# Kernel optimization log

Hardware: AMD Instinct MI355X
Metric: run time of the kernel (lower is better)

The kernel has to match this reference:

```python
import jax, jax.numpy as jnp
import numpy as np

DIM = 768
HEADS = 12
HEAD_DIM = DIM // HEADS
EPS = 1e-5


def _layernorm(x, w, b):
    # normalize over last axis (head_dim), affine params shape [head_dim]
    mu = jnp.mean(x, axis=-1, keepdims=True)
    var = jnp.mean(jnp.square(x - mu), axis=-1, keepdims=True)
    return (x - mu) * jax.lax.rsqrt(var + EPS) * w + b


def setup_inputs() -> dict:
    key = jax.random.key(0)
    ks = jax.random.split(key, 8)
    B, N, C = 8, 1024, DIM
    s = 1.0 / np.sqrt(C)
    return {
        "x": jax.random.normal(ks[0], (B, N, C), jnp.float32),
        "qkv_w": jax.random.normal(ks[1], (3 * C, C), jnp.float32) * s,
        "qkv_b": jnp.zeros((3 * C,), jnp.float32),
        "qn_w": jnp.ones((HEAD_DIM,), jnp.float32),
        "qn_b": jnp.zeros((HEAD_DIM,), jnp.float32),
        "kn_w": jnp.ones((HEAD_DIM,), jnp.float32),
        "kn_b": jnp.zeros((HEAD_DIM,), jnp.float32),
        "proj_w": jax.random.normal(ks[2], (C, C), jnp.float32) * s,
        "proj_b": jnp.zeros((C,), jnp.float32),
    }


def reference(x, qkv_w, qkv_b, qn_w, qn_b, kn_w, kn_b, proj_w, proj_b):
    B, N, C = x.shape
    H, D = HEADS, HEAD_DIM
    scale = D ** -0.5
    # qkv projection: [B,N,3C] -> [3,B,H,N,D]
    qkv = (x @ qkv_w.T + qkv_b).reshape(B, N, 3, H, D).transpose(2, 0, 3, 1, 4)
    q, k, v = qkv[0], qkv[1], qkv[2]
    q = _layernorm(q, qn_w, qn_b)
    k = _layernorm(k, kn_w, kn_b)
    # attention scores [B,H,N,N]
    attn = jnp.einsum("bhqd,bhkd->bhqk", q, k) * scale
    attn = jax.nn.softmax(attn, axis=-1)
    out = jnp.einsum("bhqk,bhkd->bhqd", attn, v)  # [B,H,N,D]
    out = out.transpose(0, 2, 1, 3).reshape(B, N, C)
    return out @ proj_w.T + proj_b
```

## Files before the change

### kernel.cpp

```cpp
#include <hip/hip_runtime.h>

#define DIM 768
#define HEADS 12
#define HDIM 64
#define B_ 8
#define N_ 1024
#define EPS 1e-5f
#define QPRE 0.18033688f

typedef __bf16 bf16x8 __attribute__((ext_vector_type(8)));
typedef float  f32x4  __attribute__((ext_vector_type(4)));

using u16 = unsigned short;
using u32 = unsigned int;

static __device__ __forceinline__ u16 f2b_rne(float f){
    u32 u = __float_as_uint(f);
    u += 0x7fffu + ((u >> 16) & 1u);
    return (u16)(u >> 16);
}

static __device__ __forceinline__ u32 cvt_pk_bf16(float lo, float hi){
    u32 r;
    asm("v_cvt_pk_bf16_f32 %0, %1, %2" : "=v"(r) : "v"(lo), "v"(hi));
    return r;
}

static __device__ __forceinline__ void gl_lds16(const void* g, void* l){
    __builtin_amdgcn_global_load_lds(
        (const __attribute__((address_space(1))) unsigned int*)g,
        (__attribute__((address_space(3))) unsigned int*)l, 16, 0, 0);
}

__global__ __launch_bounds__(256) void cast3_kernel(
    const float* __restrict__ s0, u16* __restrict__ d0, int n0,
    const float* __restrict__ s1, u16* __restrict__ d1, int n1,
    const float* __restrict__ s2, u16* __restrict__ d2, int n2)
{
    int i = blockIdx.x * 256 + threadIdx.x;
    const float* s; u16* d;
    if (i < n0)            { s = s0; d = d0; }
    else if (i < n0 + n1)  { s = s1; d = d1; i -= n0; }
    else if (i < n0+n1+n2) { s = s2; d = d2; i -= n0 + n1; }
    else return;
    const float4* p = (const float4*)s;
    float4 a = p[2*i], b = p[2*i+1];
    uint4 r;
    r.x = (u32)f2b_rne(a.x) | ((u32)f2b_rne(a.y) << 16);
    r.y = (u32)f2b_rne(a.z) | ((u32)f2b_rne(a.w) << 16);
    r.z = (u32)f2b_rne(b.x) | ((u32)f2b_rne(b.y) << 16);
    r.w = (u32)f2b_rne(b.z) | ((u32)f2b_rne(b.w) << 16);
    ((uint4*)d)[i] = r;
}

__global__ __launch_bounds__(256) void qkv_gemm_ln(
    const u16* __restrict__ xb, const u16* __restrict__ wb,
    const float* __restrict__ bias,
    const float* __restrict__ qn_w, const float* __restrict__ qn_b,
    const float* __restrict__ kn_w, const float* __restrict__ kn_b,
    u16* __restrict__ Q, u16* __restrict__ K, u16* __restrict__ VT)
{
    __shared__ __align__(16) unsigned char Asl[2][128*128];
    __shared__ __align__(16) unsigned char Bsl[2][128*128];
    const int t = threadIdx.x;
    const int lane = t & 63, wid = t >> 6;
    const int wr = wid >> 1, wc = wid & 1;
    const int l15 = lane & 15, l4 = lane >> 4;
    const int lr  = lane >> 3;
    const int lcs = ((lane & 7) ^ lr & 7) * 16;
    const int rsw = (l15 & 7) << 4;

    const int b0 = blockIdx.x;
    const int lg = (b0 & 7) * 144 + (b0 >> 3);
    const int col0 = (lg % 18) * 128, row0 = (lg / 18) * 128;

    f32x4 acc[4][4];
    #pragma unroll
    for (int m = 0; m < 4; ++m)
        #pragma unroll
        for (int n = 0; n < 4; ++n) acc[m][n] = f32x4{0.f,0.f,0.f,0.f};

    const unsigned char* aSrc = (const unsigned char*)xb + (size_t)(row0 + lr)*1536 + lcs;
    const unsigned char* bSrc = (const unsigned char*)wb + (size_t)(col0 + lr)*1536 + lcs;

    auto stage = [&](int buf, int k0s){
        #pragma unroll
        for (int c = 0; c < 4; ++c) {
            int rg = wid*32 + c*8;
            gl_lds16(aSrc + (size_t)rg*1536 + k0s*2, Asl[buf] + rg*128);
            gl_lds16(bSrc + (size_t)rg*1536 + k0s*2, Bsl[buf] + rg*128);
        }
    };

    stage(0, 0);

    for (int step = 0; step < 12; ++step) {
        const int cur = step & 1;
        if (step < 11) {
            stage(cur ^ 1, (step + 1) * 64);
            asm volatile("s_waitcnt vmcnt(8)" ::: "memory");
        } else {
            asm volatile("s_waitcnt vmcnt(0)" ::: "memory");
        }
        __builtin_amdgcn_s_barrier();

        #pragma unroll
        for (int s = 0; s < 2; ++s) {
            bf16x8 af[4], bfr[4];
            #pragma unroll
            for (int m = 0; m < 4; ++m)
                af[m] = *(const bf16x8*)(Asl[cur] + (wr*64 + m*16 + l15)*128 + ((l4*16 + s*64) ^ rsw));
            #pragma unroll
            for (int n = 0; n < 4; ++n)
                bfr[n] = *(const bf16x8*)(Bsl[cur] + (wc*64 + n*16 + l15)*128 + ((l4*16 + s*64) ^ rsw));
            #pragma unroll
            for (int m = 0; m < 4; ++m)
                #pragma unroll
                for (int n = 0; n < 4; ++n)
                    acc[m][n] = __builtin_amdgcn_mfma_f32_16x16x32_bf16(af[m], bfr[n], acc[m][n], 0, 0, 0);
        }
        __builtin_amdgcn_s_barrier();
    }

    const int cg0 = col0 + wc*64;
    const int which = cg0 / DIM;
    const int h = (cg0 % DIM) / HDIM;

    float bias_v[4];
    #pragma unroll
    for (int n = 0; n < 4; ++n) bias_v[n] = bias[cg0 + n*16 + l15];
    #pragma unroll
    for (int m = 0; m < 4; ++m)
        #pragma unroll
        for (int n = 0; n < 4; ++n)
            #pragma unroll
            for (int r = 0; r < 4; ++r) acc[m][n][r] += bias_v[n];

    unsigned char* Tw = &Asl[0][0] + wid * 8192;

    if (which < 2) {
        const float* lwp = (which == 0) ? qn_w : kn_w;
        const float* lbp = (which == 0) ? qn_b : kn_b;
        const float qsc = (which == 0) ? QPRE : 1.0f;
        float lw_v[4], lb_v[4];
        #pragma unroll
        for (int n = 0; n < 4; ++n) { lw_v[n] = lwp[n*16 + l15] * qsc; lb_v[n] = lbp[n*16 + l15] * qsc; }

        #pragma unroll
        for (int m = 0; m < 4; ++m)
            #pragma unroll
            for (int r = 0; r < 4; ++r) {
                float s = 0.f, s2 = 0.f;
                #pragma unroll
                for (int n = 0; n < 4; ++n) { float v = acc[m][n][r]; s += v; s2 += v*v; }
                #pragma unroll
                for (int off = 1; off < 16; off <<= 1) {
                    s  += __shfl_xor(s,  off, 64);
                    s2 += __shfl_xor(s2, off, 64);
                }
                float mu  = s * (1.f/64.f);
                float var = s2 * (1.f/64.f) - mu*mu;
                float rs  = rsqrtf(var + EPS);
                #pragma unroll
                for (int n = 0; n < 4; ++n)
                    acc[m][n][r] = (acc[m][n][r] - mu) * rs * lw_v[n] + lb_v[n];
            }

        #pragma unroll
        for (int m = 0; m < 4; ++m)
            #pragma unroll
            for (int n = 0; n < 4; ++n)
                #pragma unroll
                for (int r = 0; r < 4; ++r)
                    *(u16*)(Tw + (m*16 + l4*4 + r)*128 + (n*16 + l15)*2) = f2b_rne(acc[m][n][r]);

        u16* dst = (which == 0) ? Q : K;
        const int tok0 = row0 + wr*64;
        const int b = tok0 >> 10, n0 = tok0 & 1023;
        const size_t bh = (size_t)(b * HEADS + h);
        #pragma unroll
        for (int i = 0; i < 8; ++i) {
            int row = i*8 + (lane >> 3);
            int d0  = (lane & 7) * 8;
            uint4 val = *(const uint4*)(Tw + row*128 + d0*2);
            *(uint4*)(dst + (bh * N_ + n0 + row) * HDIM + d0) = val;
        }
    } else {
        #pragma unroll
        for (int n = 0; n < 4; ++n)
            #pragma unroll
            for (int m = 0; m < 4; ++m)
                #pragma unroll
                for (int r = 0; r < 4; ++r)
                    *(u16*)(Tw + (n*16 + l15)*128 + (m*16 + l4*4 + r)*2) = f2b_rne(acc[m][n][r]);

        const int tok0 = row0 + wr*64;
        const int b = tok0 >> 10, n0v = tok0 & 1023;
        const size_t bh = (size_t)(b * HEADS + h);
        #pragma unroll
        for (int i = 0; i < 8; ++i) {
            int d  = i*8 + (lane >> 3);
            int tk = (lane & 7) * 8;
            uint4 val = *(const uint4*)(Tw + d*128 + tk*2);
            *(uint4*)(VT + (bh * HDIM + d) * N_ + n0v + tk) = val;
        }
    }
}

__global__ __launch_bounds__(256) void attn_mfma(
    const u16* __restrict__ Q, const u16* __restrict__ K,
    const u16* __restrict__ VT, u16* __restrict__ A)
{
    __shared__ __align__(16) unsigned char Ks[2][64*128];
    __shared__ __align__(16) unsigned char Vs[2][64*128];
    __shared__ __align__(16) unsigned char Ps[4*2176];
    const int t = threadIdx.x, lane = t & 63, w = t >> 6;
    const int l15 = lane & 15, l4 = lane >> 4;
    const int lr  = lane >> 3;
    const int lcs = ((lane & 7) ^ lr & 7) * 16;
    const int rsw = (l15 & 7) << 4;
    const int psw = (l15 & 7) << 4;

    const int b0 = blockIdx.x;
    const int lg = (b0 & 7) * 192 + (b0 >> 3);
    const int qt = lg & 15, bh = lg >> 4;
    const size_t base = (size_t)bh * (N_ * HDIM);

    bf16x8 qa[2];
    {
        const unsigned char* qb = (const unsigned char*)(Q + base + (size_t)(qt*64 + w*16 + l15) * HDIM);
        qa[0] = *(const bf16x8*)(qb + l4*16);
        qa[1] = *(const bf16x8*)(qb + l4*16 + 64);
    }

    float l_run = 0.f;
    f32x4 o[4];
    #pragma unroll
    for (int m = 0; m < 4; ++m) o[m] = f32x4{0.f,0.f,0.f,0.f};

    unsigned char* Pw = Ps + w*2176;

    const unsigned char* kSrc = (const unsigned char*)K  + base*2 + (size_t)(w*16 + lr)*128  + lcs;
    const unsigned char* vSrc = (const unsigned char*)VT + base*2 + (size_t)(w*16 + lr)*2048 + lcs;
    unsigned char* kDst0 = Ks[0] + w*16*128;
    unsigned char* vDst0 = Vs[0] + w*16*128;

    auto stage = [&](int buf, int kt2){
        #pragma unroll
        for (int c = 0; c < 2; ++c) {
            gl_lds16(kSrc + (size_t)kt2*8192 + c*1024,  kDst0 + buf*8192 + c*1024);
            gl_lds16(vSrc + kt2*128 + c*16384,          vDst0 + buf*8192 + c*1024);
        }
    };

    stage(0, 0);

    for (int kt = 0; kt < 16; ++kt) {
        const int cur = kt & 1;
        if (kt < 15) {
            stage(cur ^ 1, kt + 1);
            asm volatile("s_waitcnt vmcnt(4)" ::: "memory");
        } else {
            asm volatile("s_waitcnt vmcnt(0)" ::: "memory");
        }
        __builtin_amdgcn_s_barrier();

        f32x4 sv[4];
        __builtin_amdgcn_s_setprio(1);
        #pragma unroll
        for (int n = 0; n < 4; ++n) {
            sv[n] = f32x4{0.f,0.f,0.f,0.f};
            #pragma unroll
            for (int s = 0; s < 2; ++s) {
                bf16x8 kb = *(const bf16x8*)(Ks[cur] + (n*16 + l15)*128 + ((l4*16 + s*64) ^ rsw));
                sv[n] = __builtin_amdgcn_mfma_f32_16x16x32_bf16(kb, qa[s], sv[n], 0, 0, 0);
            }
        }
        __builtin_amdgcn_s_setprio(0);

        #pragma unroll
        for (int n = 0; n < 4; ++n) {
            float p0 = exp2f(sv[n][0]), p1 = exp2f(sv[n][1]);
            float p2 = exp2f(sv[n][2]), p3 = exp2f(sv[n][3]);
            l_run += (p0 + p1) + (p2 + p3);
            uint2 pw;
            pw.x = cvt_pk_bf16(p0, p1);
            pw.y = cvt_pk_bf16(p2, p3);
            *(uint2*)(Pw + l15*128 + ((n*32 + l4*8) ^ psw)) = pw;
        }

        __builtin_amdgcn_s_setprio(1);
        #pragma unroll
        for (int s = 0; s < 2; ++s) {
            bf16x8 pb = *(const bf16x8*)(Pw + l15*128 + ((s*64 + l4*16) ^ psw));
            #pragma unroll
            for (int m = 0; m < 4; ++m) {
                bf16x8 vb = *(const bf16x8*)(Vs[cur] + (m*16 + l15)*128 + ((l4*16 + s*64) ^ rsw));
                o[m] = __builtin_amdgcn_mfma_f32_16x16x32_bf16(vb, pb, o[m], 0, 0, 0);
            }
        }
        __builtin_amdgcn_s_setprio(0);

        __builtin_amdgcn_s_barrier();
    }

    l_run += __shfl_xor(l_run, 16, 64);
    l_run += __shfl_xor(l_run, 32, 64);
    const float inv = 1.f / l_run;

    const int b = bh / HEADS, h = bh % HEADS;
    #pragma unroll
    for (int m = 0; m < 4; ++m)
        #pragma unroll
        for (int r = 0; r < 4; ++r)
            *(u16*)(Pw + l15*132 + (m*16 + l4*4 + r)*2) = f2b_rne(o[m][r] * inv);
    #pragma unroll
    for (int i = 0; i < 2; ++i) {
        int row = i*8 + (lane >> 3);
        int d0  = (lane & 7) * 8;
        uint4 val = *(const uint4*)(Pw + row*132 + d0*2);
        int tok = qt*64 + w*16 + row;
        *(uint4*)(A + (((size_t)b * N_ + tok) * HEADS + h) * HDIM + d0) = val;
    }
}

__global__ __launch_bounds__(256) void proj_gemm(
    const u16* __restrict__ Ab, const u16* __restrict__ wb,
    const float* __restrict__ bias, float* __restrict__ out)
{
    __shared__ __align__(16) unsigned char Asl[2][128*128];
    __shared__ __align__(16) unsigned char Bsl[2][128*128];
    const int t = threadIdx.x;
    const int lane = t & 63, wid = t >> 6;
    const int wr = wid >> 1, wc = wid & 1;
    const int l15 = lane & 15, l4 = lane >> 4;
    const int lr  = lane >> 3;
    const int lcs = ((lane & 7) ^ lr & 7) * 16;
    const int rsw = (l15 & 7) << 4;

    const int b0 = blockIdx.x;
    const int lg = (b0 & 7) * 48 + (b0 >> 3);
    const int col0 = (lg % 6) * 128, row0 = (lg / 6) * 128;

    f32x4 acc[4][4];
    #pragma unroll
    for (int m = 0; m < 4; ++m)
        #pragma unroll
        for (int n = 0; n < 4; ++n) acc[m][n] = f32x4{0.f,0.f,0.f,0.f};

    const unsigned char* aSrc = (const unsigned char*)Ab + (size_t)(row0 + lr)*1536 + lcs;
    const unsigned char* bSrc = (const unsigned char*)wb + (size_t)(col0 + lr)*1536 + lcs;

    auto stage = [&](int buf, int k0s){
        #pragma unroll
        for (int c = 0; c < 4; ++c) {
            int rg = wid*32 + c*8;
            gl_lds16(aSrc + (size_t)rg*1536 + k0s*2, Asl[buf] + rg*128);
            gl_lds16(bSrc + (size_t)rg*1536 + k0s*2, Bsl[buf] + rg*128);
        }
    };

    stage(0, 0);

    for (int step = 0; step < 12; ++step) {
        const int cur = step & 1;
        if (step < 11) {
            stage(cur ^ 1, (step + 1) * 64);
            asm volatile("s_waitcnt vmcnt(8)" ::: "memory");
        } else {
            asm volatile("s_waitcnt vmcnt(0)" ::: "memory");
        }
        __builtin_amdgcn_s_barrier();

        #pragma unroll
        for (int s = 0; s < 2; ++s) {
            bf16x8 af[4], bfr[4];
            #pragma unroll
            for (int m = 0; m < 4; ++m)
                af[m] = *(const bf16x8*)(Asl[cur] + (wr*64 + m*16 + l15)*128 + ((l4*16 + s*64) ^ rsw));
            #pragma unroll
            for (int n = 0; n < 4; ++n)
                bfr[n] = *(const bf16x8*)(Bsl[cur] + (wc*64 + n*16 + l15)*128 + ((l4*16 + s*64) ^ rsw));
            #pragma unroll
            for (int m = 0; m < 4; ++m)
                #pragma unroll
                for (int n = 0; n < 4; ++n)
                    acc[m][n] = __builtin_amdgcn_mfma_f32_16x16x32_bf16(af[m], bfr[n], acc[m][n], 0, 0, 0);
        }
        __builtin_amdgcn_s_barrier();
    }

    float bias_v[4];
    #pragma unroll
    for (int n = 0; n < 4; ++n) bias_v[n] = bias[col0 + wc*64 + n*16 + l15];
    #pragma unroll
    for (int m = 0; m < 4; ++m)
        #pragma unroll
        for (int r = 0; r < 4; ++r) {
            int rg = row0 + wr*64 + m*16 + l4*4 + r;
            #pragma unroll
            for (int n = 0; n < 4; ++n)
                out[(size_t)rg * DIM + col0 + wc*64 + n*16 + l15] = acc[m][n][r] + bias_v[n];
        }
}

extern "C" void kernel_launch(void* const* d_in, const int* in_sizes, int n_in,
                              void* d_out, int out_size, void* d_ws, size_t ws_size,
                              hipStream_t stream)
{
    const float* x      = (const float*)d_in[0];
    const float* qkv_w  = (const float*)d_in[1];
    const float* qkv_b  = (const float*)d_in[2];
    const float* qn_w   = (const float*)d_in[3];
    const float* qn_b   = (const float*)d_in[4];
    const float* kn_w   = (const float*)d_in[5];
    const float* kn_b   = (const float*)d_in[6];
    const float* proj_w = (const float*)d_in[7];
    const float* proj_b = (const float*)d_in[8];
    float* out = (float*)d_out;

    const size_t XE  = (size_t)B_ * N_ * DIM;
    const size_t QWE = (size_t)3 * DIM * DIM;
    const size_t PWE = (size_t)DIM * DIM;

    u16* xb  = (u16*)d_ws;
    u16* qwb = xb  + XE;
    u16* pwb = qwb + QWE;
    u16* Qb  = pwb + PWE;
    u16* Kb  = Qb  + XE;
    u16* VTb = Kb  + XE;
    u16* Ab  = VTb + XE;

    const int n0 = (int)(XE/8), n1 = (int)(QWE/8), n2 = (int)(PWE/8);
    cast3_kernel<<<(n0 + n1 + n2 + 255)/256, 256, 0, stream>>>(x, xb, n0, qkv_w, qwb, n1, proj_w, pwb, n2);

    qkv_gemm_ln<<<dim3(1152), 256, 0, stream>>>(xb, qwb, qkv_b, qn_w, qn_b,
                                                kn_w, kn_b, Qb, Kb, VTb);
    attn_mfma<<<dim3(1536), 256, 0, stream>>>(Qb, Kb, VTb, Ab);
    proj_gemm<<<dim3(384), 256, 0, stream>>>(Ab, pwb, proj_b, out);
}
```

Measured before the change: 137.3 us.

## Process two 16-row query groups per wave in attention to reuse K/V tiles

```diff
diff --git a/kernel.cpp b/kernel.cpp
--- a/kernel.cpp
+++ b/kernel.cpp
@@ -213,7 +213,7 @@
 {
     __shared__ __align__(16) unsigned char Ks[2][64*128];
     __shared__ __align__(16) unsigned char Vs[2][64*128];
-    __shared__ __align__(16) unsigned char Ps[4*2176];
+    __shared__ __align__(16) unsigned char Ps[4*4352];
     const int t = threadIdx.x, lane = t & 63, w = t >> 6;
     const int l15 = lane & 15, l4 = lane >> 4;
     const int lr  = lane >> 3;
@@ -222,23 +222,26 @@
     const int psw = (l15 & 7) << 4;
 
     const int b0 = blockIdx.x;
-    const int lg = (b0 & 7) * 192 + (b0 >> 3);
-    const int qt = lg & 15, bh = lg >> 4;
+    const int lg = (b0 & 7) * 96 + (b0 >> 3);
+    const int qt = lg & 7, bh = lg >> 3;
     const size_t base = (size_t)bh * (N_ * HDIM);
 
-    bf16x8 qa[2];
-    {
-        const unsigned char* qb = (const unsigned char*)(Q + base + (size_t)(qt*64 + w*16 + l15) * HDIM);
-        qa[0] = *(const bf16x8*)(qb + l4*16);
-        qa[1] = *(const bf16x8*)(qb + l4*16 + 64);
-    }
-
-    float l_run = 0.f;
-    f32x4 o[4];
-    #pragma unroll
-    for (int m = 0; m < 4; ++m) o[m] = f32x4{0.f,0.f,0.f,0.f};
-
-    unsigned char* Pw = Ps + w*2176;
+    bf16x8 qa[2][2];
+    #pragma unroll
+    for (int qg = 0; qg < 2; ++qg) {
+        const unsigned char* qb = (const unsigned char*)(Q + base + (size_t)(qt*128 + w*32 + qg*16 + l15) * HDIM);
+        qa[qg][0] = *(const bf16x8*)(qb + l4*16);
+        qa[qg][1] = *(const bf16x8*)(qb + l4*16 + 64);
+    }
+
+    float l_run[2] = {0.f, 0.f};
+    f32x4 o[2][4];
+    #pragma unroll
+    for (int qg = 0; qg < 2; ++qg)
+        #pragma unroll
+        for (int m = 0; m < 4; ++m) o[qg][m] = f32x4{0.f,0.f,0.f,0.f};
+
+    unsigned char* Pw = Ps + w*4352;
 
     const unsigned char* kSrc = (const unsigned char*)K  + base*2 + (size_t)(w*16 + lr)*128  + lcs;
     const unsigned char* vSrc = (const unsigned char*)VT + base*2 + (size_t)(w*16 + lr)*2048 + lcs;
@@ -265,38 +268,44 @@
         }
         __builtin_amdgcn_s_barrier();
 
-        f32x4 sv[4];
+        f32x4 sv[2][4];
         __builtin_amdgcn_s_setprio(1);
         #pragma unroll
         for (int n = 0; n < 4; ++n) {
-            sv[n] = f32x4{0.f,0.f,0.f,0.f};
+            sv[0][n] = f32x4{0.f,0.f,0.f,0.f};
+            sv[1][n] = f32x4{0.f,0.f,0.f,0.f};
             #pragma unroll
             for (int s = 0; s < 2; ++s) {
                 bf16x8 kb = *(const bf16x8*)(Ks[cur] + (n*16 + l15)*128 + ((l4*16 + s*64) ^ rsw));
-                sv[n] = __builtin_amdgcn_mfma_f32_16x16x32_bf16(kb, qa[s], sv[n], 0, 0, 0);
+                sv[0][n] = __builtin_amdgcn_mfma_f32_16x16x32_bf16(kb, qa[0][s], sv[0][n], 0, 0, 0);
+                sv[1][n] = __builtin_amdgcn_mfma_f32_16x16x32_bf16(kb, qa[1][s], sv[1][n], 0, 0, 0);
             }
         }
         __builtin_amdgcn_s_setprio(0);
 
         #pragma unroll
-        for (int n = 0; n < 4; ++n) {
-            float p0 = exp2f(sv[n][0]), p1 = exp2f(sv[n][1]);
-            float p2 = exp2f(sv[n][2]), p3 = exp2f(sv[n][3]);
-            l_run += (p0 + p1) + (p2 + p3);
-            uint2 pw;
-            pw.x = cvt_pk_bf16(p0, p1);
-            pw.y = cvt_pk_bf16(p2, p3);
-            *(uint2*)(Pw + l15*128 + ((n*32 + l4*8) ^ psw)) = pw;
-        }
+        for (int qg = 0; qg < 2; ++qg)
+            #pragma unroll
+            for (int n = 0; n < 4; ++n) {
+                float p0 = exp2f(sv[qg][n][0]), p1 = exp2f(sv[qg][n][1]);
+                float p2 = exp2f(sv[qg][n][2]), p3 = exp2f(sv[qg][n][3]);
+                l_run[qg] += (p0 + p1) + (p2 + p3);
+                uint2 pw;
+                pw.x = cvt_pk_bf16(p0, p1);
+                pw.y = cvt_pk_bf16(p2, p3);
+                *(uint2*)(Pw + (qg*16 + l15)*128 + ((n*32 + l4*8) ^ psw)) = pw;
+            }
 
         __builtin_amdgcn_s_setprio(1);
         #pragma unroll
         for (int s = 0; s < 2; ++s) {
-            bf16x8 pb = *(const bf16x8*)(Pw + l15*128 + ((s*64 + l4*16) ^ psw));
+            bf16x8 pb0 = *(const bf16x8*)(Pw + (l15)*128      + ((s*64 + l4*16) ^ psw));
+            bf16x8 pb1 = *(const bf16x8*)(Pw + (16 + l15)*128 + ((s*64 + l4*16) ^ psw));
             #pragma unroll
             for (int m = 0; m < 4; ++m) {
                 bf16x8 vb = *(const bf16x8*)(Vs[cur] + (m*16 + l15)*128 + ((l4*16 + s*64) ^ rsw));
-                o[m] = __builtin_amdgcn_mfma_f32_16x16x32_bf16(vb, pb, o[m], 0, 0, 0);
+                o[0][m] = __builtin_amdgcn_mfma_f32_16x16x32_bf16(vb, pb0, o[0][m], 0, 0, 0);
+                o[1][m] = __builtin_amdgcn_mfma_f32_16x16x32_bf16(vb, pb1, o[1][m], 0, 0, 0);
             }
         }
         __builtin_amdgcn_s_setprio(0);
@@ -304,22 +313,27 @@
         __builtin_amdgcn_s_barrier();
     }
 
-    l_run += __shfl_xor(l_run, 16, 64);
-    l_run += __shfl_xor(l_run, 32, 64);
-    const float inv = 1.f / l_run;
+    #pragma unroll
+    for (int qg = 0; qg < 2; ++qg) {
+        l_run[qg] += __shfl_xor(l_run[qg], 16, 64);
+        l_run[qg] += __shfl_xor(l_run[qg], 32, 64);
+    }
+    const float inv0 = 1.f / l_run[0], inv1 = 1.f / l_run[1];
 
     const int b = bh / HEADS, h = bh % HEADS;
     #pragma unroll
     for (int m = 0; m < 4; ++m)
         #pragma unroll
-        for (int r = 0; r < 4; ++r)
-            *(u16*)(Pw + l15*132 + (m*16 + l4*4 + r)*2) = f2b_rne(o[m][r] * inv);
-    #pragma unroll
-    for (int i = 0; i < 2; ++i) {
+        for (int r = 0; r < 4; ++r) {
+            *(u16*)(Pw + l15*132        + (m*16 + l4*4 + r)*2) = f2b_rne(o[0][m][r] * inv0);
+            *(u16*)(Pw + (16 + l15)*132 + (m*16 + l4*4 + r)*2) = f2b_rne(o[1][m][r] * inv1);
+        }
+    #pragma unroll
+    for (int i = 0; i < 4; ++i) {
         int row = i*8 + (lane >> 3);
         int d0  = (lane & 7) * 8;
         uint4 val = *(const uint4*)(Pw + row*132 + d0*2);
-        int tok = qt*64 + w*16 + row;
+        int tok = qt*128 + w*32 + row;
         *(uint4*)(A + (((size_t)b * N_ + tok) * HEADS + h) * HDIM + d0) = val;
     }
 }
@@ -436,6 +450,6 @@
 
     qkv_gemm_ln<<<dim3(1152), 256, 0, stream>>>(xb, qwb, qkv_b, qn_w, qn_b,
                                                 kn_w, kn_b, Qb, Kb, VTb);
-    attn_mfma<<<dim3(1536), 256, 0, stream>>>(Qb, Kb, VTb, Ab);
+    attn_mfma<<<dim3(768), 256, 0, stream>>>(Qb, Kb, VTb, Ab);
     proj_gemm<<<dim3(384), 256, 0, stream>>>(Ab, pwb, proj_b, out);
 }
```

Result: faster. 131.8 us (median of 3 runs) (-4.0%).
